# Kernel optimization log

Hardware: AMD Instinct MI355X
Metric: run time of the kernel (lower is better)

The kernel has to match this reference:

```python
import jax, jax.numpy as jnp
import numpy as np

NUM_USERS = 100_000
NUM_ITEMS = 50_000
EMBED_DIM = 64
NUM_LAYERS = 3
NUM_BASE_EDGES = 2_000_000
BATCH = 4096


def setup_inputs() -> dict:
    key = jax.random.key(0)
    k_ue, k_ie, k_u, k_i, k_uid, k_iid = jax.random.split(key, 6)
    N = NUM_USERS + NUM_ITEMS
    # learned embedding tables (std=0.01 init as in the torch module)
    user_emb = 0.01 * jax.random.normal(k_ue, (NUM_USERS, EMBED_DIM), dtype=jnp.float32)
    item_emb = 0.01 * jax.random.normal(k_ie, (NUM_ITEMS, EMBED_DIM), dtype=jnp.float32)
    # random bipartite interaction edges (u, v); symmetrized as in _build_graph
    u = jax.random.randint(k_u, (NUM_BASE_EDGES,), 0, NUM_USERS, dtype=jnp.int32)
    v = jax.random.randint(k_i, (NUM_BASE_EDGES,), 0, NUM_ITEMS, dtype=jnp.int32) + NUM_USERS
    rows = jnp.concatenate([u, v])  # [2E]
    cols = jnp.concatenate([v, u])  # [2E]
    # symmetric degree normalization: A_hat[r,c] = 1 / (sqrt(deg[r]) * sqrt(deg[c]))
    deg = jax.ops.segment_sum(jnp.ones_like(rows, dtype=jnp.float32), rows, num_segments=N)
    sqrt_deg = jnp.sqrt(deg)
    vals = 1.0 / (sqrt_deg[rows] * sqrt_deg[cols])
    user_ids = jax.random.randint(k_uid, (BATCH,), 0, NUM_USERS, dtype=jnp.int32)
    item_ids = jax.random.randint(k_iid, (BATCH,), 0, NUM_ITEMS, dtype=jnp.int32)
    return {
        "user_emb": user_emb,
        "item_emb": item_emb,
        "vals": vals,
        "rows": rows,
        "cols": cols,
        "user_ids": user_ids,
        "item_ids": item_ids,
    }


def _spmm(vals, rows, cols, x, num_segments):
    # COO SpMM: out[r] += vals[e] * x[cols[e]]  (irregular gather + scatter-add)
    return jax.ops.segment_sum(vals[:, None] * x[cols], rows, num_segments=num_segments)


def reference(user_emb, item_emb, vals, rows, cols, user_ids, item_ids):
    num_users = user_emb.shape[0]
    N = num_users + item_emb.shape[0]
    all_emb = jnp.concatenate([user_emb, item_emb], axis=0)  # [N, D]
    acc = jnp.zeros_like(all_emb)
    for _ in range(NUM_LAYERS):  # eval mode: no stochastic noise injection
        all_emb = _spmm(vals, rows, cols, all_emb, N)
        acc = acc + all_emb
    final = acc / NUM_LAYERS  # mean over layer outputs
    u = final[user_ids]                       # [B, D]
    i = final[item_ids + num_users]           # [B, D]
    return (u * i).sum(axis=-1)               # [B]
```

## Files before the change

### kernel.cpp

```cpp
#include <hip/hip_runtime.h>


#define EMBED_DIM 64
#define NUM_LAYERS 3
#define RSHIFT 8
#define RMASK 255
#define NBMAX 640
#define CAPU 8192
#define CAPI 12288
#define TP 4096
#define OUT_CAP 12288

__device__ __forceinline__ int bucket_base(int b, int BSPLIT) {
    int lo = (b < BSPLIT) ? b : BSPLIT;
    int hi = (b > BSPLIT) ? (b - BSPLIT) : 0;
    return lo * CAPU + hi * CAPI;
}


__device__ __forceinline__ unsigned bf16pair(float a, float b) {
    unsigned ia = __float_as_uint(a);
    unsigned ib = __float_as_uint(b);
    ia = (ia + 0x7fffu + ((ia >> 16) & 1u)) >> 16;
    ib = (ib + 0x7fffu + ((ib >> 16) & 1u)) & 0xffff0000u;
    return ia | ib;
}
__device__ __forceinline__ float bf_lo(unsigned u) { return __uint_as_float(u << 16); }
__device__ __forceinline__ float bf_hi(unsigned u) { return __uint_as_float(u & 0xffff0000u); }


__global__ __launch_bounds__(512) void split_kernel(const int* __restrict__ uu,
                                                    const int* __restrict__ vv,
                                                    int* __restrict__ gcur,
                                                    int* __restrict__ bin, int E2, int NB,
                                                    int BSPLIT) {
    __shared__ int h[NBMAX], exl[NBMAX], curb[NBMAX], gb[NBMAX];
    __shared__ int wp[8];
    __shared__ int stage[2 * TP];
    int tid = threadIdx.x;
    int lane = tid & 63, wid = tid >> 6;
    for (int i = tid; i < NB; i += 512) h[i] = 0;
    __syncthreads();
    int e0 = blockIdx.x * TP, e1 = min(e0 + TP, E2);
    int j = e0 + tid * 4;
    for (; j + 3 < e1; j += 2048) {
        int4 u4 = *(const int4*)(uu + j);
        int4 v4 = *(const int4*)(vv + j);
        atomicAdd(&h[u4.x >> RSHIFT], 1); atomicAdd(&h[v4.x >> RSHIFT], 1);
        atomicAdd(&h[u4.y >> RSHIFT], 1); atomicAdd(&h[v4.y >> RSHIFT], 1);
        atomicAdd(&h[u4.z >> RSHIFT], 1); atomicAdd(&h[v4.z >> RSHIFT], 1);
        atomicAdd(&h[u4.w >> RSHIFT], 1); atomicAdd(&h[v4.w >> RSHIFT], 1);
    }
    for (; j < e1; ++j) {
        atomicAdd(&h[uu[j] >> RSHIFT], 1);
        atomicAdd(&h[vv[j] >> RSHIFT], 1);
    }
    __syncthreads();
    {
        int b2 = tid * 2;
        int v0 = (b2     < NB) ? h[b2]     : 0;
        int v1 = (b2 + 1 < NB) ? h[b2 + 1] : 0;
        int tsum = v0 + v1;
        int x = tsum;
        for (int off = 1; off < 64; off <<= 1) {
            int y = __shfl_up(x, off, 64);
            if (lane >= off) x += y;
        }
        if (lane == 63) wp[wid] = x;
        __syncthreads();
        int wadd = 0;
        for (int k = 0; k < wid; ++k) wadd += wp[k];
        int tpre = wadd + x - tsum;
        if (b2     < NB) exl[b2]     = tpre;
        if (b2 + 1 < NB) exl[b2 + 1] = tpre + v0;
        __syncthreads();
    }
    for (int b = tid; b < NB; b += 512) {
        curb[b] = exl[b];
        gb[b]   = h[b] ? (bucket_base(b, BSPLIT) + atomicAdd(&gcur[b], h[b])) : 0;
    }
    __syncthreads();
    j = e0 + tid * 4;
    for (; j + 3 < e1; j += 2048) {
        int4 u4 = *(const int4*)(uu + j);
        int4 v4 = *(const int4*)(vv + j);
        int p;
        p = atomicAdd(&curb[u4.x >> RSHIFT], 1); stage[p] = (v4.x << RSHIFT) | (u4.x & RMASK);
        p = atomicAdd(&curb[v4.x >> RSHIFT], 1); stage[p] = (u4.x << RSHIFT) | (v4.x & RMASK);
        p = atomicAdd(&curb[u4.y >> RSHIFT], 1); stage[p] = (v4.y << RSHIFT) | (u4.y & RMASK);
        p = atomicAdd(&curb[v4.y >> RSHIFT], 1); stage[p] = (u4.y << RSHIFT) | (v4.y & RMASK);
        p = atomicAdd(&curb[u4.z >> RSHIFT], 1); stage[p] = (v4.z << RSHIFT) | (u4.z & RMASK);
        p = atomicAdd(&curb[v4.z >> RSHIFT], 1); stage[p] = (u4.z << RSHIFT) | (v4.z & RMASK);
        p = atomicAdd(&curb[u4.w >> RSHIFT], 1); stage[p] = (v4.w << RSHIFT) | (u4.w & RMASK);
        p = atomicAdd(&curb[v4.w >> RSHIFT], 1); stage[p] = (u4.w << RSHIFT) | (v4.w & RMASK);
    }
    for (; j < e1; ++j) {
        int u = uu[j], v = vv[j];
        int p1 = atomicAdd(&curb[u >> RSHIFT], 1);
        stage[p1] = (v << RSHIFT) | (u & RMASK);
        int p2 = atomicAdd(&curb[v >> RSHIFT], 1);
        stage[p2] = (u << RSHIFT) | (v & RMASK);
    }
    __syncthreads();
    int noct = tid >> 3, osub = tid & 7;
    for (int b = noct; b < NB; b += 64) {
        int cnt_b = h[b];
        int st = exl[b], g = gb[b];
        for (int k = osub; k < cnt_b; k += 8) bin[g + k] = stage[st + k];
    }
}


__global__ __launch_bounds__(512) void csr_kernel(const int* __restrict__ bin,
                                                  const int* __restrict__ gcur,
                                                  int* __restrict__ row_ptr,
                                                  int* __restrict__ deg,
                                                  int* __restrict__ col_idx,
                                                  const float4* __restrict__ ue,
                                                  const float4* __restrict__ ie,
                                                  unsigned* __restrict__ w0x,
                                                  int N, int U, int BSPLIT) {
    __shared__ int h2[256], cur2[256];
    __shared__ float rs2[256];
    __shared__ int wp[8];
    __shared__ __align__(16) int outst[OUT_CAP];
    int b   = blockIdx.x;
    int tid = threadIdx.x;
    int lane = tid & 63, wid = tid >> 6;
    int s = bucket_base(b, BSPLIT);
    int cnt = gcur[b];
    if (tid < 256) h2[tid] = 0;
    __syncthreads();
    int cnt4 = cnt >> 2;
    const int4* bin4 = (const int4*)(bin + s);
    for (int j = tid; j < cnt4; j += 512) {
        int4 v = bin4[j];
        atomicAdd(&h2[v.x & RMASK], 1);
        atomicAdd(&h2[v.y & RMASK], 1);
        atomicAdd(&h2[v.z & RMASK], 1);
        atomicAdd(&h2[v.w & RMASK], 1);
    }
    for (int j = (cnt4 << 2) + tid; j < cnt; j += 512) atomicAdd(&h2[bin[s + j] & RMASK], 1);
    __syncthreads();
    int myh = (tid < 256) ? h2[tid] : 0;
    if (tid < 256) rs2[tid] = (myh > 0) ? rsqrtf((float)myh) : 0.0f;
    {
        int x = myh;
        for (int off = 1; off < 64; off <<= 1) {
            int y = __shfl_up(x, off, 64);
            if (lane >= off) x += y;
        }
        if (lane == 63) wp[wid] = x;
        __syncthreads();
        if (tid < 256) {
            int wadd = 0;
            for (int k = 0; k < wid; ++k) wadd += wp[k];
            cur2[tid] = wadd + x - myh;
        }
    }
    int gr = (b << RSHIFT) + tid;
    if (tid < 256 && gr < N) {
        row_ptr[gr] = s + ((tid < 256) ? 0 : 0);
    }
    __syncthreads();
    if (tid < 256 && gr < N) {
        row_ptr[gr] = s + cur2[tid];
        deg[gr]     = myh;
    }
    if (cnt <= OUT_CAP) {
        for (int j = tid; j < cnt4; j += 512) {
            int4 v = bin4[j];
            int p;
            p = atomicAdd(&cur2[v.x & RMASK], 1); outst[p] = v.x >> RSHIFT;
            p = atomicAdd(&cur2[v.y & RMASK], 1); outst[p] = v.y >> RSHIFT;
            p = atomicAdd(&cur2[v.z & RMASK], 1); outst[p] = v.z >> RSHIFT;
            p = atomicAdd(&cur2[v.w & RMASK], 1); outst[p] = v.w >> RSHIFT;
        }
        for (int j = (cnt4 << 2) + tid; j < cnt; j += 512) {
            int v = bin[s + j];
            int p = atomicAdd(&cur2[v & RMASK], 1);
            outst[p] = v >> RSHIFT;
        }
        __syncthreads();
        int4* dst4 = (int4*)(col_idx + s);
        for (int j = tid; j < cnt4; j += 512) dst4[j] = ((const int4*)outst)[j];
        for (int j = (cnt4 << 2) + tid; j < cnt; j += 512) col_idx[s + j] = outst[j];
    } else {
        for (int j = tid; j < cnt; j += 512) {
            int v = bin[s + j];
            int p = atomicAdd(&cur2[v & RMASK], 1);
            col_idx[s + p] = v >> RSHIFT;
        }
    }
    for (int idx = tid; idx < 256 * 16; idx += 512) {
        int rl = idx >> 4, sub = idx & 15;
        int n = (b << RSHIFT) + rl;
        if (n < N) {
            float4 v = (n < U) ? ue[(size_t)n * 16 + sub] : ie[(size_t)(n - U) * 16 + sub];
            float rs = rs2[rl];
            uint2 o;
            o.x = bf16pair(v.x * rs, v.y * rs);
            o.y = bf16pair(v.z * rs, v.w * rs);
            ((uint2*)w0x)[(size_t)n * 16 + sub] = o;
        }
    }
}


__global__ __launch_bounds__(256) void spmm_kernel(const int* __restrict__ row_ptr,
                                                   const int* __restrict__ deg,
                                                   const int* __restrict__ col_idx,
                                                   const uint4* __restrict__ x4,
                                                   uint4* __restrict__ y4, int N) {
    int gw   = (blockIdx.x * blockDim.x + threadIdx.x) >> 6;
    int lane = threadIdx.x & 63;
    int oct  = lane >> 3, sub = lane & 7;
    int r = gw * 8 + oct;
    if (r >= N) return;
    int s = row_ptr[r];
    int d = deg[r];
    float2 a0 = {0, 0}, a1 = {0, 0}, a2 = {0, 0}, a3 = {0, 0};
    int k = 0;
    for (; k + 3 < d; k += 4) {
        int c0 = col_idx[s + k];
        int c1 = col_idx[s + k + 1];
        int c2 = col_idx[s + k + 2];
        int c3 = col_idx[s + k + 3];
        uint4 u0 = x4[(size_t)c0 * 8 + sub];
        uint4 u1 = x4[(size_t)c1 * 8 + sub];
        uint4 u2 = x4[(size_t)c2 * 8 + sub];
        uint4 u3 = x4[(size_t)c3 * 8 + sub];
        a0.x += bf_lo(u0.x); a0.y += bf_hi(u0.x);
        a1.x += bf_lo(u0.y); a1.y += bf_hi(u0.y);
        a2.x += bf_lo(u0.z); a2.y += bf_hi(u0.z);
        a3.x += bf_lo(u0.w); a3.y += bf_hi(u0.w);
        a0.x += bf_lo(u1.x); a0.y += bf_hi(u1.x);
        a1.x += bf_lo(u1.y); a1.y += bf_hi(u1.y);
        a2.x += bf_lo(u1.z); a2.y += bf_hi(u1.z);
        a3.x += bf_lo(u1.w); a3.y += bf_hi(u1.w);
        a0.x += bf_lo(u2.x); a0.y += bf_hi(u2.x);
        a1.x += bf_lo(u2.y); a1.y += bf_hi(u2.y);
        a2.x += bf_lo(u2.z); a2.y += bf_hi(u2.z);
        a3.x += bf_lo(u2.w); a3.y += bf_hi(u2.w);
        a0.x += bf_lo(u3.x); a0.y += bf_hi(u3.x);
        a1.x += bf_lo(u3.y); a1.y += bf_hi(u3.y);
        a2.x += bf_lo(u3.z); a2.y += bf_hi(u3.z);
        a3.x += bf_lo(u3.w); a3.y += bf_hi(u3.w);
    }
    for (; k < d; ++k) {
        int c0 = col_idx[s + k];
        uint4 u0 = x4[(size_t)c0 * 8 + sub];
        a0.x += bf_lo(u0.x); a0.y += bf_hi(u0.x);
        a1.x += bf_lo(u0.y); a1.y += bf_hi(u0.y);
        a2.x += bf_lo(u0.z); a2.y += bf_hi(u0.z);
        a3.x += bf_lo(u0.w); a3.y += bf_hi(u0.w);
    }
    float inv = (d > 0) ? (1.0f / (float)d) : 0.0f;
    uint4 o;
    o.x = bf16pair(a0.x * inv, a0.y * inv);
    o.y = bf16pair(a1.x * inv, a1.y * inv);
    o.z = bf16pair(a2.x * inv, a2.y * inv);
    o.w = bf16pair(a3.x * inv, a3.y * inv);
    y4[(size_t)r * 8 + sub] = o;
}


__global__ __launch_bounds__(256) void batch_readout_kernel(const int* __restrict__ row_ptr,
                                                            const int* __restrict__ deg,
                                                            const int* __restrict__ col_idx,
                                                            const uint4* __restrict__ x4,
                                                            const uint4* __restrict__ l1,
                                                            const uint4* __restrict__ l2,
                                                            const int* __restrict__ user_ids,
                                                            const int* __restrict__ item_ids,
                                                            float* __restrict__ out,
                                                            int B, int U) {
    __shared__ float sm[16][8][8];
    __shared__ float dsm[16];
    int tid = threadIdx.x;
    int oct = tid >> 3, sub = tid & 7;
    int pair = oct & 15, is_item = oct >> 4;
    int b = blockIdx.x * 16 + pair;
    bool active = (b < B);
    float sv[8];
#pragma unroll
    for (int k = 0; k < 8; ++k) sv[k] = 0.0f;
    float dd = 0.0f;
    if (active) {
        int r = is_item ? (item_ids[b] + U) : user_ids[b];
        int s = row_ptr[r];
        int d = deg[r];
        dd = (float)d;
        float2 a0 = {0, 0}, a1 = {0, 0}, a2 = {0, 0}, a3 = {0, 0};
        int k = 0;
        for (; k + 3 < d; k += 4) {
            int c0 = col_idx[s + k];
            int c1 = col_idx[s + k + 1];
            int c2 = col_idx[s + k + 2];
            int c3 = col_idx[s + k + 3];
            uint4 u0 = x4[(size_t)c0 * 8 + sub];
            uint4 u1 = x4[(size_t)c1 * 8 + sub];
            uint4 u2 = x4[(size_t)c2 * 8 + sub];
            uint4 u3 = x4[(size_t)c3 * 8 + sub];
            a0.x += bf_lo(u0.x); a0.y += bf_hi(u0.x);
            a1.x += bf_lo(u0.y); a1.y += bf_hi(u0.y);
            a2.x += bf_lo(u0.z); a2.y += bf_hi(u0.z);
            a3.x += bf_lo(u0.w); a3.y += bf_hi(u0.w);
            a0.x += bf_lo(u1.x); a0.y += bf_hi(u1.x);
            a1.x += bf_lo(u1.y); a1.y += bf_hi(u1.y);
            a2.x += bf_lo(u1.z); a2.y += bf_hi(u1.z);
            a3.x += bf_lo(u1.w); a3.y += bf_hi(u1.w);
            a0.x += bf_lo(u2.x); a0.y += bf_hi(u2.x);
            a1.x += bf_lo(u2.y); a1.y += bf_hi(u2.y);
            a2.x += bf_lo(u2.z); a2.y += bf_hi(u2.z);
            a3.x += bf_lo(u2.w); a3.y += bf_hi(u2.w);
            a0.x += bf_lo(u3.x); a0.y += bf_hi(u3.x);
            a1.x += bf_lo(u3.y); a1.y += bf_hi(u3.y);
            a2.x += bf_lo(u3.z); a2.y += bf_hi(u3.z);
            a3.x += bf_lo(u3.w); a3.y += bf_hi(u3.w);
        }
        for (; k < d; ++k) {
            int c0 = col_idx[s + k];
            uint4 u0 = x4[(size_t)c0 * 8 + sub];
            a0.x += bf_lo(u0.x); a0.y += bf_hi(u0.x);
            a1.x += bf_lo(u0.y); a1.y += bf_hi(u0.y);
            a2.x += bf_lo(u0.z); a2.y += bf_hi(u0.z);
            a3.x += bf_lo(u0.w); a3.y += bf_hi(u0.w);
        }
        float inv = (d > 0) ? (1.0f / (float)d) : 0.0f;
        uint4 u1v = l1[(size_t)r * 8 + sub];
        uint4 u2v = l2[(size_t)r * 8 + sub];
        sv[0] = bf_lo(u1v.x) + bf_lo(u2v.x) + a0.x * inv;
        sv[1] = bf_hi(u1v.x) + bf_hi(u2v.x) + a0.y * inv;
        sv[2] = bf_lo(u1v.y) + bf_lo(u2v.y) + a1.x * inv;
        sv[3] = bf_hi(u1v.y) + bf_hi(u2v.y) + a1.y * inv;
        sv[4] = bf_lo(u1v.z) + bf_lo(u2v.z) + a2.x * inv;
        sv[5] = bf_hi(u1v.z) + bf_hi(u2v.z) + a2.y * inv;
        sv[6] = bf_lo(u1v.w) + bf_lo(u2v.w) + a3.x * inv;
        sv[7] = bf_hi(u1v.w) + bf_hi(u2v.w) + a3.y * inv;
    }
    if (is_item) {
#pragma unroll
        for (int k = 0; k < 8; ++k) sm[pair][sub][k] = sv[k];
        if (sub == 0) dsm[pair] = dd;
    }
    __syncthreads();
    if (!is_item && active) {
        float p = 0.0f;
#pragma unroll
        for (int k = 0; k < 8; ++k) p += sv[k] * sm[pair][sub][k];
#pragma unroll
        for (int off = 4; off > 0; off >>= 1) p += __shfl_down(p, off, 8);
        if (sub == 0) {
            float du = dd;
            float di = dsm[pair];
            out[b] = p * sqrtf(du) * sqrtf(di) * (1.0f / (NUM_LAYERS * NUM_LAYERS));
        }
    }
}


extern "C" void kernel_launch(void* const* d_in, const int* in_sizes, int n_in,
                              void* d_out, int out_size, void* d_ws, size_t ws_size,
                              hipStream_t stream) {
    const float* user_emb = (const float*)d_in[0];
    const float* item_emb = (const float*)d_in[1];
    const int*   rows     = (const int*)d_in[3];
    const int*   cols     = (const int*)d_in[4];
    const int*   user_ids = (const int*)d_in[5];
    const int*   item_ids = (const int*)d_in[6];
    float*       out      = (float*)d_out;

    const int U = in_sizes[0] / EMBED_DIM;
    const int I = in_sizes[1] / EMBED_DIM;
    const int E2 = in_sizes[3] >> 1;
    const int B = in_sizes[5];
    const int N = U + I;
    const int NB = (N + RMASK) >> RSHIFT;
    const int BSPLIT = U >> RSHIFT;

    const long long TOT = (long long)((NB < BSPLIT ? NB : BSPLIT)) * CAPU +
                          (long long)((NB > BSPLIT) ? (NB - BSPLIT) : 0) * CAPI;

    char* w = (char*)d_ws;
    unsigned* x2      = (unsigned*)w; w += (size_t)N * 32 * sizeof(unsigned);
    unsigned* L1      = (unsigned*)w; w += (size_t)N * 32 * sizeof(unsigned);
    unsigned* L2      = (unsigned*)w; w += (size_t)N * 32 * sizeof(unsigned);
    int*      bin     = (int*)w;      w += (size_t)TOT * sizeof(int);
    int*      col_idx = (int*)w;      w += (size_t)TOT * sizeof(int);
    int*      row_ptr = (int*)w;      w += (size_t)N * sizeof(int);
    int*      deg     = (int*)w;      w += (size_t)N * sizeof(int);
    int*      gcur    = (int*)w;      w += (size_t)NB * sizeof(int);

    const int GP = (E2 + TP - 1) / TP;

    hipMemsetAsync(gcur, 0, (size_t)NB * sizeof(int), stream);
    split_kernel<<<GP, 512, 0, stream>>>(rows, cols, gcur, bin, E2, NB, BSPLIT);
    csr_kernel<<<NB, 512, 0, stream>>>(bin, gcur, row_ptr, deg, col_idx,
                                       (const float4*)user_emb, (const float4*)item_emb,
                                       x2, N, U, BSPLIT);

    const int T = 256;
    const int GS = (N * 8 + T - 1) / T;
    spmm_kernel<<<GS, T, 0, stream>>>(row_ptr, deg, col_idx,
                                      (const uint4*)x2, (uint4*)L1, N);
    spmm_kernel<<<GS, T, 0, stream>>>(row_ptr, deg, col_idx,
                                      (const uint4*)L1, (uint4*)L2, N);

    batch_readout_kernel<<<(B + 15) / 16, T, 0, stream>>>(row_ptr, deg, col_idx,
                                                          (const uint4*)L2,
                                                          (const uint4*)L1, (const uint4*)L2,
                                                          user_ids, item_ids, out, B, U);
}
```

Baseline: 288.1 us.

## Drop LDS staging in CSR build, reorder buckets, shrink readout blocks

The CSR kernel no longer stages column indices in a 48KB shared buffer before copying them out. It scatters them straight to global memory, which frees LDS and should raise occupancy, at the cost of uncoalesced writes. Blocks now process the larger item buckets first to reduce the tail. The split kernel tile size changes, and the readout kernel runs 128-thread blocks handling 8 pairs each to spread the small batch over more CUs.

```diff
diff --git a/kernel.cpp b/kernel.cpp
--- a/kernel.cpp
+++ b/kernel.cpp
@@ -8,8 +8,7 @@
 #define NBMAX 640
 #define CAPU 8192
 #define CAPI 12288
-#define TP 4096
-#define OUT_CAP 12288
+#define TP 3584
 
 __device__ __forceinline__ int bucket_base(int b, int BSPLIT) {
     int lo = (b < BSPLIT) ? b : BSPLIT;
@@ -119,12 +118,13 @@
                                                   const float4* __restrict__ ue,
                                                   const float4* __restrict__ ie,
                                                   unsigned* __restrict__ w0x,
-                                                  int N, int U, int BSPLIT) {
+                                                  int N, int U, int BSPLIT, int NB) {
     __shared__ int h2[256], cur2[256];
     __shared__ float rs2[256];
     __shared__ int wp[8];
-    __shared__ __align__(16) int outst[OUT_CAP];
-    int b   = blockIdx.x;
+    int nbi = NB - BSPLIT;
+    int bb  = blockIdx.x;
+    int b   = (bb < nbi) ? (BSPLIT + bb) : (bb - nbi);
     int tid = threadIdx.x;
     int lane = tid & 63, wid = tid >> 6;
     int s = bucket_base(b, BSPLIT);
@@ -160,37 +160,22 @@
     }
     int gr = (b << RSHIFT) + tid;
     if (tid < 256 && gr < N) {
-        row_ptr[gr] = s + ((tid < 256) ? 0 : 0);
-    }
-    __syncthreads();
-    if (tid < 256 && gr < N) {
         row_ptr[gr] = s + cur2[tid];
         deg[gr]     = myh;
     }
-    if (cnt <= OUT_CAP) {
-        for (int j = tid; j < cnt4; j += 512) {
-            int4 v = bin4[j];
-            int p;
-            p = atomicAdd(&cur2[v.x & RMASK], 1); outst[p] = v.x >> RSHIFT;
-            p = atomicAdd(&cur2[v.y & RMASK], 1); outst[p] = v.y >> RSHIFT;
-            p = atomicAdd(&cur2[v.z & RMASK], 1); outst[p] = v.z >> RSHIFT;
-            p = atomicAdd(&cur2[v.w & RMASK], 1); outst[p] = v.w >> RSHIFT;
-        }
-        for (int j = (cnt4 << 2) + tid; j < cnt; j += 512) {
-            int v = bin[s + j];
-            int p = atomicAdd(&cur2[v & RMASK], 1);
-            outst[p] = v >> RSHIFT;
-        }
-        __syncthreads();
-        int4* dst4 = (int4*)(col_idx + s);
-        for (int j = tid; j < cnt4; j += 512) dst4[j] = ((const int4*)outst)[j];
-        for (int j = (cnt4 << 2) + tid; j < cnt; j += 512) col_idx[s + j] = outst[j];
-    } else {
-        for (int j = tid; j < cnt; j += 512) {
-            int v = bin[s + j];
-            int p = atomicAdd(&cur2[v & RMASK], 1);
-            col_idx[s + p] = v >> RSHIFT;
-        }
+    __syncthreads();
+    for (int j = tid; j < cnt4; j += 512) {
+        int4 v = bin4[j];
+        int p;
+        p = atomicAdd(&cur2[v.x & RMASK], 1); col_idx[s + p] = v.x >> RSHIFT;
+        p = atomicAdd(&cur2[v.y & RMASK], 1); col_idx[s + p] = v.y >> RSHIFT;
+        p = atomicAdd(&cur2[v.z & RMASK], 1); col_idx[s + p] = v.z >> RSHIFT;
+        p = atomicAdd(&cur2[v.w & RMASK], 1); col_idx[s + p] = v.w >> RSHIFT;
+    }
+    for (int j = (cnt4 << 2) + tid; j < cnt; j += 512) {
+        int v = bin[s + j];
+        int p = atomicAdd(&cur2[v & RMASK], 1);
+        col_idx[s + p] = v >> RSHIFT;
     }
     for (int idx = tid; idx < 256 * 16; idx += 512) {
         int rl = idx >> 4, sub = idx & 15;
@@ -265,7 +250,7 @@
 }
 
 
-__global__ __launch_bounds__(256) void batch_readout_kernel(const int* __restrict__ row_ptr,
+__global__ __launch_bounds__(128) void batch_readout_kernel(const int* __restrict__ row_ptr,
                                                             const int* __restrict__ deg,
                                                             const int* __restrict__ col_idx,
                                                             const uint4* __restrict__ x4,
@@ -275,12 +260,12 @@
                                                             const int* __restrict__ item_ids,
                                                             float* __restrict__ out,
                                                             int B, int U) {
-    __shared__ float sm[16][8][8];
-    __shared__ float dsm[16];
+    __shared__ float sm[8][8][8];
+    __shared__ float dsm[8];
     int tid = threadIdx.x;
     int oct = tid >> 3, sub = tid & 7;
-    int pair = oct & 15, is_item = oct >> 4;
-    int b = blockIdx.x * 16 + pair;
+    int pair = oct & 7, is_item = oct >> 3;
+    int b = blockIdx.x * 8 + pair;
     bool active = (b < B);
     float sv[8];
 #pragma unroll
@@ -398,7 +383,7 @@
     split_kernel<<<GP, 512, 0, stream>>>(rows, cols, gcur, bin, E2, NB, BSPLIT);
     csr_kernel<<<NB, 512, 0, stream>>>(bin, gcur, row_ptr, deg, col_idx,
                                        (const float4*)user_emb, (const float4*)item_emb,
-                                       x2, N, U, BSPLIT);
+                                       x2, N, U, BSPLIT, NB);
 
     const int T = 256;
     const int GS = (N * 8 + T - 1) / T;
@@ -407,7 +392,7 @@
     spmm_kernel<<<GS, T, 0, stream>>>(row_ptr, deg, col_idx,
                                       (const uint4*)L1, (uint4*)L2, N);
 
-    batch_readout_kernel<<<(B + 15) / 16, T, 0, stream>>>(row_ptr, deg, col_idx,
+    batch_readout_kernel<<<(B + 7) / 8, 128, 0, stream>>>(row_ptr, deg, col_idx,
                                                           (const uint4*)L2,
                                                           (const uint4*)L1, (const uint4*)L2,
                                                           user_ids, item_ids, out, B, U);
```

Result: slower. 310.7 us (+7.8%).
